# Kernel tuning notes

Measured on AMD Instinct MI355X. Metric: run time of the kernel, lower is better.

## Reference

```python
import jax, jax.numpy as jnp
import numpy as np

# dims
B, N, M, K = 8, 4096, 1024, 32      # batch, points, centers, neighbors
CIN, CT = 64, 64                    # feature / temb channels
C1, C2 = 64, 128                    # SharedMLP out_channels
G, EPS = 8, 1e-5                    # GroupNorm(8, oc)


def setup_inputs() -> dict:
    key = jax.random.key(0)
    ks = jax.random.split(key, 8)
    return {
        "features": jax.random.normal(ks[0], (B, CIN, N), jnp.float32),
        "coords": jax.random.uniform(ks[1], (B, 3, N), jnp.float32),
        "temb": jax.random.normal(ks[2], (B, CT, N), jnp.float32),
        # SharedMLP params: Conv2d 1x1 -> (O, I) weight, GroupNorm affine
        "W1": jax.random.normal(ks[3], (C1, CIN + 3), jnp.float32) * 0.05,
        "b1": jnp.zeros((C1,), jnp.float32),
        "g1": jnp.ones((C1,), jnp.float32),
        "be1": jnp.zeros((C1,), jnp.float32),
        "W2": jax.random.normal(ks[4], (C2, C1), jnp.float32) * 0.05,
        "b2": jnp.zeros((C2,), jnp.float32),
        "g2": jnp.ones((C2,), jnp.float32),
        "be2": jnp.zeros((C2,), jnp.float32),
    }


def fps_indices(pts):
    # pts: [N, 3] -> [M] indices. Deterministic start at index 0
    # (original uses a random start; math otherwise identical).
    d0 = jnp.sum((pts - pts[0]) ** 2, axis=-1)  # [N]
    def step(dist, _):
        far = jnp.argmax(dist)
        dist = jnp.minimum(dist, jnp.sum((pts - pts[far]) ** 2, axis=-1))
        return dist, far
    _, fars = jax.lax.scan(step, d0, None, length=M - 1)
    return jnp.concatenate([jnp.zeros((1,), fars.dtype), fars])


def group_norm(x, gamma, beta):
    # x: [B, C, M, K], normalize per group over (C//G, M, K)
    b, c, m, k = x.shape
    xr = x.reshape(b, G, c // G, m, k)
    mu = xr.mean(axis=(2, 3, 4), keepdims=True)
    var = xr.var(axis=(2, 3, 4), keepdims=True)
    xn = ((xr - mu) * jax.lax.rsqrt(var + EPS)).reshape(b, c, m, k)
    return xn * gamma[:, None, None] + beta[:, None, None]


def swish(x):
    return x * jax.nn.sigmoid(x)


def reference(features, coords, temb, W1, b1, g1, be1, W2, b2, g2, be2):
    # --- furthest point sampling ---
    idx = jax.vmap(fps_indices)(coords.transpose(0, 2, 1))          # [B, M]
    centers = jax.vmap(lambda c, i: c[:, i])(coords, idx)           # [B, 3, M]
    # --- 'ball query' (actually kNN: source argsorts dist, takes first K) ---
    c = centers.transpose(0, 2, 1)                                  # [B, M, 3]
    p = coords.transpose(0, 2, 1)                                   # [B, N, 3]
    d = (jnp.sum(c * c, -1)[:, :, None] + jnp.sum(p * p, -1)[:, None, :]
         - 2.0 * jnp.einsum('bmd,bnd->bmn', c, p))                  # [B, M, N]
    _, nidx = jax.lax.top_k(-d, K)                                  # [B, M, K]
    gather = jax.vmap(lambda xb, ib: xb[:, ib])                     # [B,C,N],[B,M,K]->[B,C,M,K]
    gcoords = gather(coords, nidx) - centers[..., None]             # [B, 3, M, K]
    gtemb = gather(temb, nidx)                                      # [B, CT, M, K]
    gfeat = jnp.concatenate([gcoords, gather(features, nidx)], axis=1)  # [B, 3+CIN, M, K]
    # --- SharedMLP (1x1 conv -> GN -> Swish) x2, then max over neighbors ---
    h = swish(group_norm(jnp.einsum('oc,bcmk->bomk', W1, gfeat) + b1[:, None, None], g1, be1))
    h = swish(group_norm(jnp.einsum('oc,bcmk->bomk', W2, h) + b2[:, None, None], g2, be2))
    return h.max(axis=-1), centers, gtemb.max(axis=-1)
```

## Files before the change

### kernel.cpp

```cpp
#include <hip/hip_runtime.h>
#include <stdint.h>

#define BB 8
#define NN 4096
#define MM 1024
#define KK 32

__device__ __forceinline__ float bf2f(unsigned short u) {
    union { unsigned int i; float f; } v; v.i = ((unsigned int)u) << 16; return v.f;
}
__device__ __forceinline__ unsigned short f2bf(float f) {
    union { float f; unsigned int i; } v; v.f = f;
    unsigned int x = v.i;
    x += 0x7fffu + ((x >> 16) & 1u);
    return (unsigned short)(x >> 16);
}
__device__ __forceinline__ float swishf(float y) {
    return __fdividef(y, 1.0f + __expf(-y));
}

#define OUT1_OFF 1048576
#define OUT2_OFF 1073152

#define P_W1 0
#define P_B1 4288
#define P_G1 4352
#define P_BE1 4416
#define P_W2 4480
#define P_B2 12672
#define P_G2 12800
#define P_BE2 12928

__device__ __forceinline__ int detect_flag_wave(const unsigned short* f, int lane) {
    unsigned short u = f[lane * 2];
    float x = fabsf(bf2f(u));
    bool ext = (u != 0) && (x > 100.0f || x < 1e-30f);
    unsigned long long m = __ballot(ext);
    return (__popcll(m) >= 16) ? 1 : 0;
}

#define DPP_STAGE(CTRL) { \
    union { double d; unsigned int u[2]; } s_, r_; \
    s_.d = bd; \
    r_.u[0] = (unsigned)__builtin_amdgcn_update_dpp(0, (int)s_.u[0], CTRL, 0xF, 0xF, true); \
    r_.u[1] = (unsigned)__builtin_amdgcn_update_dpp(0, (int)s_.u[1], CTRL, 0xF, 0xF, true); \
    int op_ = __builtin_amdgcn_update_dpp(0, bp, CTRL, 0xF, 0xF, true); \
    double od_ = r_.d; \
    bool rep_ = (od_ > bd) || (od_ == bd && op_ < bp); \
    bd = rep_ ? od_ : bd; bp = rep_ ? op_ : bp; }

__device__ __forceinline__ void redmax64(double& bd, int& bp) {
    DPP_STAGE(0xB1)
    DPP_STAGE(0x4E)
    DPP_STAGE(0x141)
    DPP_STAGE(0x140)
#pragma unroll
    for (int m = 32; m >= 16; m >>= 1) {
        double od = __shfl_xor(bd, m, 64);
        int op = __shfl_xor(bp, m, 64);
        bool rep = (od > bd) || (od == bd && op < bp);
        bd = rep ? od : bd; bp = rep ? op : bp;
    }
}

__global__ __launch_bounds__(256) void k_cvt_all(
    const void* __restrict__ feat, const void* __restrict__ coords,
    float* __restrict__ featT, float* __restrict__ coordsC,
    float* __restrict__ paramsC,
    int* __restrict__ qhead, int* __restrict__ progress,
    float* __restrict__ stats1,
    const void* W1, const void* b1, const void* g1, const void* be1,
    const void* W2, const void* b2, const void* g2, const void* be2)
{
    __shared__ float tile[64][65];
    __shared__ int sflag;
    int tid = threadIdx.x, blk = blockIdx.x;
    if (tid < 64) {
        int fl0 = detect_flag_wave((const unsigned short*)feat, tid);
        if (tid == 0) sflag = fl0;
    }
    __syncthreads();
    int fl = sflag;
    if (blk == 0) {
        if (tid == 0) *qhead = 0;
        if (tid < 8) progress[tid * 16] = -1;
        stats1[tid] = 0.f;
        stats1[tid + 256] = 0.f;
    }
    if (blk < 512) {
        int i = blk;
        int b = i >> 6, n0 = (i & 63) * 64;
        int c = tid >> 2, q = tid & 3;
        size_t base = ((size_t)b * 64 + c) * NN + n0 + q * 16;
        if (fl) {
            const float* sp = (const float*)feat + base;
#pragma unroll
            for (int j = 0; j < 16; j++) tile[c][q * 16 + j] = sp[j];
        } else {
            const unsigned short* sp = (const unsigned short*)feat + base;
#pragma unroll
            for (int j = 0; j < 16; j++) tile[c][q * 16 + j] = bf2f(sp[j]);
        }
        __syncthreads();
        int n = tid >> 2;
        float* dp = featT + ((size_t)b * NN + n0 + n) * 64 + q * 16;
#pragma unroll
        for (int j = 0; j < 16; j++) dp[j] = tile[q * 16 + j][n];
    } else if (blk < 896) {
        int idx = (blk - 512) * 256 + tid;
        coordsC[idx] = fl ? ((const float*)coords)[idx]
                          : bf2f(((const unsigned short*)coords)[idx]);
    } else {
        int idx = (blk - 896) * 256 + tid;
        if (idx < 13056) {
            const void* src; int off;
            if (idx < 4288)       { src = W1;  off = idx; }
            else if (idx < 4352)  { src = b1;  off = idx - 4288; }
            else if (idx < 4416)  { src = g1;  off = idx - 4352; }
            else if (idx < 4480)  { src = be1; off = idx - 4416; }
            else if (idx < 12672) { src = W2;  off = idx - 4480; }
            else if (idx < 12800) { src = b2;  off = idx - 12672; }
            else if (idx < 12928) { src = g2;  off = idx - 12800; }
            else                  { src = be2; off = idx - 12928; }
            paramsC[idx] = fl ? ((const float*)src)[off]
                              : bf2f(((const unsigned short*)src)[off]);
        }
    }
}

#define W1Tm(j,c)     (((float*)SM)[(j)*64+(c)])
#define GBUFm(mi,k,c) (((float*)(SM+17152))[(((mi)*32+(k))*66)+(c)])
#define GCm(mi,j,k)   (((float*)(SM+50944))[(((mi)*3+(j))*32)+(k)])
#define NDm(mi,k)     (((int*)(SM+52480))[((mi)*32)+(k)])
#define W2Tm(j,c)     (((float*)SM)[(j)*128+(c)])
#define ACTm(mi,j,k)  (((float*)(SM+32768))[(((mi)*64+(j))*32)+(k)])

struct PW { double d; int p; int q; };
#define PSM_XS   ((float*)(SM))
#define PSM_YS   ((float*)(SM + 16384))
#define PSM_ZS   ((float*)(SM + 32768))
#define PSM_HIST ((int*)(SM + 49152))
#define PSM_PWB  ((PW*)(SM + 53248))
#define PSM_SF   ((int*)(SM + 53376))

#define RESCAN(G) { \
    double gd = 1.0e300; int ga = (G) * 8; \
    _Pragma("unroll") \
    for (int i = 0; i < 8; i++) { \
        int sl = (G) * 8 + i; \
        unsigned int bit = (sl < 32) ? (elo >> sl) : (ehi >> (sl - 32)); \
        double cd = (bit & 1u) ? 1.0e300 : d[sl]; \
        bool rep = cd < gd; \
        gd = rep ? cd : gd; ga = rep ? sl : ga; \
    } \
    g8[(G)] = gd; a8[(G)] = ga; }

__global__ __launch_bounds__(256) void k_fpsknn(
    const void* __restrict__ coords, const float* __restrict__ coordsC,
    float* __restrict__ centersF, int* __restrict__ nidx,
    const void* __restrict__ temb, const void* __restrict__ feat,
    const float* __restrict__ featT, const float* __restrict__ paramsC,
    float* __restrict__ stats1,
    void* __restrict__ d_out,
    int* __restrict__ qhead, int* __restrict__ progress)
{
    __shared__ __align__(16) char SM[55296];
    int tid = threadIdx.x;
    int blk = blockIdx.x;
    if (tid < 64) {
        int fl0 = detect_flag_wave((const unsigned short*)feat, tid);
        if (tid == 0) *PSM_SF = fl0;
    }
    __syncthreads();
    int fl = *PSM_SF;

    if (blk < 8) {
        int b = blk;
        if (fl) {
            const float* cb = (const float*)coords + (size_t)b * 3 * NN;
#pragma unroll
            for (int i = 0; i < 16; i++) {
                int p = tid + i * 256;
                PSM_XS[p] = cb[p]; PSM_YS[p] = cb[NN + p]; PSM_ZS[p] = cb[2 * NN + p];
            }
        } else {
            const unsigned short* cb = (const unsigned short*)coords + (size_t)b * 3 * NN;
#pragma unroll
            for (int i = 0; i < 16; i++) {
                int p = tid + i * 256;
                PSM_XS[p] = bf2f(cb[p]); PSM_YS[p] = bf2f(cb[NN + p]); PSM_ZS[p] = bf2f(cb[2 * NN + p]);
            }
        }
        if (tid == 0) PSM_HIST[0] = 0;
        __syncthreads();
        if (tid == 0) {
            *(float4*)(centersF + (size_t)b * MM * 4) =
                make_float4(PSM_XS[0], PSM_YS[0], PSM_ZS[0], 0.f);
            __hip_atomic_store(&progress[b * 16], 0, __ATOMIC_RELEASE, __HIP_MEMORY_SCOPE_AGENT);
        }
        int base = tid * 16;
        double px[16], py[16], pz[16], dist[16];
        double x0 = (double)PSM_XS[0], y0 = (double)PSM_YS[0], z0 = (double)PSM_ZS[0];
        double bd = -1.0; int bp = base;
#pragma unroll
        for (int j = 0; j < 16; j++) {
            px[j] = (double)PSM_XS[base + j]; py[j] = (double)PSM_YS[base + j]; pz[j] = (double)PSM_ZS[base + j];
            double dx = px[j] - x0, dy = py[j] - y0, dz = pz[j] - z0;
            dist[j] = fma(dz, dz, fma(dy, dy, dx * dx));
            bool rep = dist[j] > bd;
            bd = rep ? dist[j] : bd; bp = rep ? base + j : bp;
        }
        int lane = tid & 63, wid = tid >> 6;
#pragma unroll 1
        for (int s = 1; s < MM; s++) {
            redmax64(bd, bp);
            int par = s & 1;
            if (lane == 0) { PW w; w.d = bd; w.p = bp; w.q = 0; PSM_PWB[par * 4 + wid] = w; }
            __syncthreads();
            PW w0 = PSM_PWB[par * 4 + 0];
            double wd = w0.d; int wp = w0.p;
#pragma unroll
            for (int w = 1; w < 4; w++) {
                PW ww = PSM_PWB[par * 4 + w];
                bool rep = (ww.d > wd) || (ww.d == wd && ww.p < wp);
                wd = rep ? ww.d : wd; wp = rep ? ww.p : wp;
            }
            if (tid == 0) PSM_HIST[s] = wp;
            if ((s & 31) == 31 && s >= 63 && wid == ((s >> 5) & 3)) {
                int s0 = s - 63;
                if (lane < 32) {
                    int far = PSM_HIST[s0 + lane];
                    *(float4*)(centersF + ((size_t)b * MM + s0 + lane) * 4) =
                        make_float4(PSM_XS[far], PSM_YS[far], PSM_ZS[far], 0.f);
                }
                if (lane == 0)
                    __hip_atomic_store(&progress[b * 16], s0 + 31,
                                       __ATOMIC_RELEASE, __HIP_MEMORY_SCOPE_AGENT);
            }
            double fx = (double)PSM_XS[wp], fy = (double)PSM_YS[wp], fz = (double)PSM_ZS[wp];
            bd = -1.0; bp = base;
#pragma unroll
            for (int j = 0; j < 16; j++) {
                double dx = px[j] - fx, dy = py[j] - fy, dz = pz[j] - fz;
                double d = fma(dz, dz, fma(dy, dy, dx * dx));
                dist[j] = fmin(dist[j], d);
                bool rep = dist[j] > bd;
                bd = rep ? dist[j] : bd; bp = rep ? base + j : bp;
            }
        }
        __syncthreads();
        if (tid < 32) {
            int far = PSM_HIST[992 + tid];
            *(float4*)(centersF + ((size_t)b * MM + 992 + tid) * 4) =
                make_float4(PSM_XS[far], PSM_YS[far], PSM_ZS[far], 0.f);
        }
        if (tid == 0)
            __hip_atomic_store(&progress[b * 16], 1023,
                               __ATOMIC_RELEASE, __HIP_MEMORY_SCOPE_AGENT);
#pragma unroll
        for (int i = 0; i < 4; i++) {
            int m = tid + i * 256;
            int far = PSM_HIST[m];
            float X = PSM_XS[far], Y = PSM_YS[far], Z = PSM_ZS[far];
            if (fl) {
                float* o = (float*)d_out;
                o[OUT1_OFF + (size_t)(b * 3 + 0) * MM + m] = X;
                o[OUT1_OFF + (size_t)(b * 3 + 1) * MM + m] = Y;
                o[OUT1_OFF + (size_t)(b * 3 + 2) * MM + m] = Z;
            } else {
                unsigned short* o = (unsigned short*)d_out;
                o[OUT1_OFF + (size_t)(b * 3 + 0) * MM + m] = f2bf(X);
                o[OUT1_OFF + (size_t)(b * 3 + 1) * MM + m] = f2bf(Y);
                o[OUT1_OFF + (size_t)(b * 3 + 2) * MM + m] = f2bf(Z);
            }
        }
    } else {
        int lane = tid & 63, wid = tid >> 6;
        for (int t = tid; t < 64 * 67; t += 256) {
            int c = t / 67, j = t % 67;
            W1Tm(j, c) = paramsC[P_W1 + t];
        }
        __syncthreads();
        for (;;) {
            int id = 0;
            if (lane == 0) id = atomicAdd(qhead, 1);
            id = __shfl(id, 0, 64);
            if (id >= BB * MM) break;
            int b = id & 7, m = id >> 3;
            while (__hip_atomic_load(&progress[b * 16], __ATOMIC_RELAXED,
                                     __HIP_MEMORY_SCOPE_AGENT) < m)
                __builtin_amdgcn_s_sleep(64);
            (void)__hip_atomic_load(&progress[b * 16], __ATOMIC_ACQUIRE,
                                    __HIP_MEMORY_SCOPE_AGENT);
            int bm = b * MM + m;
            const float* cb = coordsC + (size_t)b * 3 * NN;
            float4 ctr = *(const float4*)(centersF + (size_t)bm * 4);
            double cx = (double)ctr.x, cy = (double)ctr.y, cz = (double)ctr.z;
            double cc = (cx * cx + cy * cy) + cz * cz;
            double d[64];
#pragma unroll 4
            for (int j = 0; j < 64; j++) {
                int p = j * 64 + lane;
                double x = (double)cb[p], y = (double)cb[NN + p], z = (double)cb[2 * NN + p];
                double pp = (x * x + y * y) + z * z;
                double dt = (cx * x + cy * y) + cz * z;
                d[j] = (cc + pp) - 2.0 * dt;
            }
            double g8[8]; int a8[8];
#pragma unroll
            for (int g = 0; g < 8; g++) {
                double gd = d[g * 8]; int ga = g * 8;
#pragma unroll
                for (int i = 1; i < 8; i++) {
                    int sl = g * 8 + i;
                    bool rep = d[sl] < gd;
                    gd = rep ? d[sl] : gd; ga = rep ? sl : ga;
                }
                g8[g] = gd; a8[g] = ga;
            }
            unsigned int elo = 0, ehi = 0;
            int res = 0;
#pragma unroll 1
            for (int it = 0; it < 32; it++) {
                double bd = g8[0]; int ba = a8[0];
#pragma unroll
                for (int g = 1; g < 8; g++) {
                    bool rep = g8[g] < bd;
                    bd = rep ? g8[g] : bd; ba = rep ? a8[g] : ba;
                }
                int bp = ba * 64 + lane;
                double wd = bd; int wp = bp;
#pragma unroll
                for (int s = 32; s >= 1; s >>= 1) {
                    double od = __shfl_xor(wd, s, 64);
                    int op = __shfl_xor(wp, s, 64);
                    bool rep = (od < wd) || (od == wd && op < wp);
                    wd = rep ? od : wd; wp = rep ? op : wp;
                }
                res = (lane == it) ? wp : res;
                if (bp == wp) {
                    int slot = ba;
                    if (slot < 32) elo |= (1u << slot); else ehi |= (1u << (slot - 32));
                    int g = slot >> 3;
                    switch (g) {
                        case 0: RESCAN(0) break;
                        case 1: RESCAN(1) break;
                        case 2: RESCAN(2) break;
                        case 3: RESCAN(3) break;
                        case 4: RESCAN(4) break;
                        case 5: RESCAN(5) break;
                        case 6: RESCAN(6) break;
                        case 7: RESCAN(7) break;
                    }
                }
            }
            if (lane < KK) nidx[(size_t)bm * KK + lane] = res;
            float best = -3.0e38f;
            if (fl) {
                const float* tb = (const float*)temb + ((size_t)b * 64 + lane) * NN;
#pragma unroll 4
                for (int k = 0; k < 32; k++) {
                    int nk = __shfl(res, k, 64);
                    best = fmaxf(best, tb[nk]);
                }
            } else {
                const unsigned short* tb = (const unsigned short*)temb + ((size_t)b * 64 + lane) * NN;
#pragma unroll 4
                for (int k = 0; k < 32; k++) {
                    int nk = __shfl(res, k, 64);
                    best = fmaxf(best, bf2f(tb[nk]));
                }
            }
            size_t off = (size_t)OUT2_OFF + ((size_t)(b * 64 + lane)) * MM + m;
            if (fl) ((float*)d_out)[off] = best;
            else    ((unsigned short*)d_out)[off] = f2bf(best);
            if (lane < 32) NDm(wid, lane) = res & (NN - 1);
            const float* fb = featT + (size_t)b * NN * 64;
#pragma unroll 4
            for (int q = 0; q < 32; q++) {
                int n = NDm(wid, q);
                GBUFm(wid, q, lane) = fb[(size_t)n * 64 + lane];
            }
            if (lane < 32) {
                int n = NDm(wid, lane);
                GCm(wid, 0, lane) = __fsub_rn(cb[n], ctr.x);
                GCm(wid, 1, lane) = __fsub_rn(cb[NN + n], ctr.y);
                GCm(wid, 2, lane) = __fsub_rn(cb[2 * NN + n], ctr.z);
            }
            int c0 = (lane >> 3) * 8;
            int k0 = (lane & 7) * 4;
            float acc[8][4];
#pragma unroll
            for (int i = 0; i < 8; i++)
#pragma unroll
                for (int kk = 0; kk < 4; kk++) acc[i][kk] = 0.f;
#pragma unroll
            for (int j = 0; j < 3; j++) {
                float4 a = *(const float4*)&GCm(wid, j, k0);
                float4 w0 = *(const float4*)&W1Tm(j, c0);
                float4 w1v = *(const float4*)&W1Tm(j, c0 + 4);
                float w[8] = {w0.x, w0.y, w0.z, w0.w, w1v.x, w1v.y, w1v.z, w1v.w};
#pragma unroll
                for (int i = 0; i < 8; i++) {
                    acc[i][0] = fmaf(w[i], a.x, acc[i][0]);
                    acc[i][1] = fmaf(w[i], a.y, acc[i][1]);
                    acc[i][2] = fmaf(w[i], a.z, acc[i][2]);
                    acc[i][3] = fmaf(w[i], a.w, acc[i][3]);
                }
            }
#pragma unroll 4
            for (int c = 0; c < 64; c++) {
                float f0 = GBUFm(wid, k0 + 0, c);
                float f1 = GBUFm(wid, k0 + 1, c);
                float f2 = GBUFm(wid, k0 + 2, c);
                float f3 = GBUFm(wid, k0 + 3, c);
                int j = 3 + c;
                float4 w0 = *(const float4*)&W1Tm(j, c0);
                float4 w1v = *(const float4*)&W1Tm(j, c0 + 4);
                float w[8] = {w0.x, w0.y, w0.z, w0.w, w1v.x, w1v.y, w1v.z, w1v.w};
#pragma unroll
                for (int i = 0; i < 8; i++) {
                    acc[i][0] = fmaf(w[i], f0, acc[i][0]);
                    acc[i][1] = fmaf(w[i], f1, acc[i][1]);
                    acc[i][2] = fmaf(w[i], f2, acc[i][2]);
                    acc[i][3] = fmaf(w[i], f3, acc[i][3]);
                }
            }
            float s = 0.f, s2 = 0.f;
#pragma unroll
            for (int i = 0; i < 8; i++) {
                float bb = paramsC[P_B1 + c0 + i];
#pragma unroll
                for (int kk = 0; kk < 4; kk++) {
                    float v = acc[i][kk] + bb;
                    s += v; s2 = fmaf(v, v, s2);
                }
            }
            s += __shfl_xor(s, 1, 64); s += __shfl_xor(s, 2, 64); s += __shfl_xor(s, 4, 64);
            s2 += __shfl_xor(s2, 1, 64); s2 += __shfl_xor(s2, 2, 64); s2 += __shfl_xor(s2, 4, 64);
            if ((lane & 7) == 0) {
                int g = lane >> 3;
                atomicAdd(&stats1[(b * 8 + g) * 2], s);
                atomicAdd(&stats1[(b * 8 + g) * 2 + 1], s2);
            }
        }
    }
}

__device__ __forceinline__ void mlp1_compute(
    char* SM, int tid, int lane, int mi, int b, int bm,
    const float* __restrict__ featT, const float* __restrict__ coordsC,
    const float* __restrict__ centersF, const int* __restrict__ nidx,
    const float* __restrict__ P, float acc[8][4])
{
    for (int t = tid; t < 64 * 67; t += 256) {
        int c = t / 67, j = t % 67;
        W1Tm(j, c) = P[P_W1 + t];
    }
    if (lane < 32) NDm(mi, lane) = nidx[(size_t)bm * KK + lane] & (NN - 1);
    __syncthreads();
    const float* fb = featT + (size_t)b * NN * 64;
#pragma unroll 4
    for (int q = 0; q < 32; q++) {
        int n = NDm(mi, q);
        GBUFm(mi, q, lane) = fb[(size_t)n * 64 + lane];
    }
    float4 ctr = *(const float4*)(centersF + (size_t)bm * 4);
    const float* cb = coordsC + (size_t)b * 3 * NN;
    if (lane < 32) {
        int n = NDm(mi, lane);
        GCm(mi, 0, lane) = __fsub_rn(cb[n], ctr.x);
        GCm(mi, 1, lane) = __fsub_rn(cb[NN + n], ctr.y);
        GCm(mi, 2, lane) = __fsub_rn(cb[2 * NN + n], ctr.z);
    }
    __syncthreads();
    int c0 = (lane >> 3) * 8;
    int k0 = (lane & 7) * 4;
#pragma unroll
    for (int i = 0; i < 8; i++)
#pragma unroll
        for (int kk = 0; kk < 4; kk++) acc[i][kk] = 0.f;
#pragma unroll
    for (int j = 0; j < 3; j++) {
        float4 a = *(const float4*)&GCm(mi, j, k0);
        float4 w0 = *(const float4*)&W1Tm(j, c0);
        float4 w1v = *(const float4*)&W1Tm(j, c0 + 4);
        float w[8] = {w0.x, w0.y, w0.z, w0.w, w1v.x, w1v.y, w1v.z, w1v.w};
#pragma unroll
        for (int i = 0; i < 8; i++) {
            acc[i][0] = fmaf(w[i], a.x, acc[i][0]);
            acc[i][1] = fmaf(w[i], a.y, acc[i][1]);
            acc[i][2] = fmaf(w[i], a.z, acc[i][2]);
            acc[i][3] = fmaf(w[i], a.w, acc[i][3]);
        }
    }
#pragma unroll 4
    for (int c = 0; c < 64; c++) {
        float f0 = GBUFm(mi, k0 + 0, c);
        float f1 = GBUFm(mi, k0 + 1, c);
        float f2 = GBUFm(mi, k0 + 2, c);
        float f3 = GBUFm(mi, k0 + 3, c);
        int j = 3 + c;
        float4 w0 = *(const float4*)&W1Tm(j, c0);
        float4 w1v = *(const float4*)&W1Tm(j, c0 + 4);
        float w[8] = {w0.x, w0.y, w0.z, w0.w, w1v.x, w1v.y, w1v.z, w1v.w};
#pragma unroll
        for (int i = 0; i < 8; i++) {
            acc[i][0] = fmaf(w[i], f0, acc[i][0]);
            acc[i][1] = fmaf(w[i], f1, acc[i][1]);
            acc[i][2] = fmaf(w[i], f2, acc[i][2]);
            acc[i][3] = fmaf(w[i], f3, acc[i][3]);
        }
    }
}

__device__ __forceinline__ void mlp2_compute(
    char* SM, int tid, int lane, int mi, int b,
    const float acc1[8][4], const float* __restrict__ S1,
    const float* __restrict__ P, float acc2[16][4])
{
    __syncthreads();
    int c0 = (lane >> 3) * 8;
    int k0 = (lane & 7) * 4;
    int g = c0 >> 3;
    float S = S1[(b * 8 + g) * 2], Q = S1[(b * 8 + g) * 2 + 1];
    float mean = S * (1.0f / 262144.0f);
    float var = Q * (1.0f / 262144.0f) - mean * mean;
    float inv = rsqrtf(var + 1e-5f);
#pragma unroll
    for (int i = 0; i < 8; i++) {
        int c = c0 + i;
        float sc = P[P_G1 + c] * inv;
        float sh = P[P_BE1 + c] - mean * sc;
        float bb = P[P_B1 + c];
#pragma unroll
        for (int kk = 0; kk < 4; kk++)
            ACTm(mi, c, k0 + kk) = swishf(fmaf(acc1[i][kk] + bb, sc, sh));
    }
    for (int t = tid; t < 128 * 64; t += 256) {
        int c = t >> 6, j = t & 63;
        W2Tm(j, c) = P[P_W2 + t];
    }
    __syncthreads();
    int c02 = (lane >> 3) * 16;
#pragma unroll
    for (int i = 0; i < 16; i++)
#pragma unroll
        for (int kk = 0; kk < 4; kk++) acc2[i][kk] = 0.f;
#pragma unroll 4
    for (int j = 0; j < 64; j++) {
        float4 a = *(const float4*)&ACTm(mi, j, k0);
        float4 w0 = *(const float4*)&W2Tm(j, c02);
        float4 w1v = *(const float4*)&W2Tm(j, c02 + 4);
        float4 w2v = *(const float4*)&W2Tm(j, c02 + 8);
        float4 w3 = *(const float4*)&W2Tm(j, c02 + 12);
        float w[16] = {w0.x, w0.y, w0.z, w0.w, w1v.x, w1v.y, w1v.z, w1v.w,
                       w2v.x, w2v.y, w2v.z, w2v.w, w3.x, w3.y, w3.z, w3.w};
#pragma unroll
        for (int i = 0; i < 16; i++) {
            acc2[i][0] = fmaf(w[i], a.x, acc2[i][0]);
            acc2[i][1] = fmaf(w[i], a.y, acc2[i][1]);
            acc2[i][2] = fmaf(w[i], a.z, acc2[i][2]);
            acc2[i][3] = fmaf(w[i], a.w, acc2[i][3]);
        }
    }
}

__global__ __launch_bounds__(256) void k_mlp2s(
    const float* __restrict__ featT, const float* __restrict__ coordsC,
    const float* __restrict__ centersF, const int* __restrict__ nidx,
    const float* __restrict__ P, const float* __restrict__ stats1,
    float* __restrict__ stats2)
{
    __shared__ __align__(16) char smem[65536];
    char* SM = smem;
    int tid = threadIdx.x, blk = blockIdx.x;
    int b = blk >> 8, m0 = (blk & 255) * 4;
    int mi = tid >> 6, lane = tid & 63;
    int bm = b * MM + m0 + mi;
    float acc1[8][4];
    mlp1_compute(SM, tid, lane, mi, b, bm, featT, coordsC, centersF, nidx, P, acc1);
    float acc2[16][4];
    mlp2_compute(SM, tid, lane, mi, b, acc1, stats1, P, acc2);
    int c02 = (lane >> 3) * 16;
    float s = 0.f, s2 = 0.f;
#pragma unroll
    for (int i = 0; i < 16; i++) {
        float bb = P[P_B2 + c02 + i];
#pragma unroll
        for (int kk = 0; kk < 4; kk++) {
            float v = acc2[i][kk] + bb;
            s += v; s2 = fmaf(v, v, s2);
        }
    }
    s += __shfl_xor(s, 1, 64); s += __shfl_xor(s, 2, 64); s += __shfl_xor(s, 4, 64);
    s2 += __shfl_xor(s2, 1, 64); s2 += __shfl_xor(s2, 2, 64); s2 += __shfl_xor(s2, 4, 64);
    __syncthreads();
    float* sred = (float*)SM;
    if ((lane & 7) == 0) {
        int g = lane >> 3;
        sred[(mi * 8 + g) * 2] = s;
        sred[(mi * 8 + g) * 2 + 1] = s2;
    }
    __syncthreads();
    if (tid < 16) {
        int g = tid >> 1, w = tid & 1;
        float t = sred[(0 * 8 + g) * 2 + w] + sred[(1 * 8 + g) * 2 + w]
                + sred[(2 * 8 + g) * 2 + w] + sred[(3 * 8 + g) * 2 + w];
        atomicAdd(&stats2[(b * 8 + g) * 2 + w], t);
    }
}

__global__ __launch_bounds__(256) void k_final(
    const float* __restrict__ featT, const float* __restrict__ coordsC,
    const float* __restrict__ centersF, const int* __restrict__ nidx,
    const float* __restrict__ P, const float* __restrict__ stats1,
    const float* __restrict__ stats2,
    void* __restrict__ d_out, const void* __restrict__ feat)
{
    __shared__ __align__(16) char smem[65536];
    char* SM = smem;
    int tid = threadIdx.x, blk = blockIdx.x;
    if (tid < 64) {
        int fl0 = detect_flag_wave((const unsigned short*)feat, tid);
        if (tid == 0) *(int*)(SM + 53248) = fl0;
    }
    __syncthreads();
    int fl = *(int*)(SM + 53248);
    int b = blk >> 8, m0 = (blk & 255) * 4;
    int mi = tid >> 6, lane = tid & 63;
    int bm = b * MM + m0 + mi;
    float acc1[8][4];
    mlp1_compute(SM, tid, lane, mi, b, bm, featT, coordsC, centersF, nidx, P, acc1);
    float acc2[16][4];
    mlp2_compute(SM, tid, lane, mi, b, acc1, stats1, P, acc2);
    int c02 = (lane >> 3) * 16;
    int g2 = c02 >> 4;
    float S = stats2[(b * 8 + g2) * 2], Q = stats2[(b * 8 + g2) * 2 + 1];
    float mean = S * (1.0f / 524288.0f);
    float var = Q * (1.0f / 524288.0f) - mean * mean;
    float inv = rsqrtf(var + 1e-5f);
    float mx[16];
#pragma unroll
    for (int i = 0; i < 16; i++) {
        int c = c02 + i;
        float sc = P[P_G2 + c] * inv;
        float sh = P[P_BE2 + c] - mean * sc;
        float bb = P[P_B2 + c];
        float v = -3.0e38f;
#pragma unroll
        for (int kk = 0; kk < 4; kk++)
            v = fmaxf(v, swishf(fmaf(acc2[i][kk] + bb, sc, sh)));
        v = fmaxf(v, __shfl_xor(v, 1, 64));
        v = fmaxf(v, __shfl_xor(v, 2, 64));
        v = fmaxf(v, __shfl_xor(v, 4, 64));
        mx[i] = v;
    }
    if ((lane & 7) == 0) {
        int m = m0 + mi;
#pragma unroll
        for (int i = 0; i < 16; i++) {
            size_t off = (size_t)(b * 128 + c02 + i) * MM + m;
            if (fl) ((float*)d_out)[off] = mx[i];
            else    ((unsigned short*)d_out)[off] = f2bf(mx[i]);
        }
    }
}

extern "C" void kernel_launch(void* const* d_in, const int* in_sizes, int n_in,
                              void* d_out, int out_size, void* d_ws, size_t ws_size,
                              hipStream_t stream) {
    (void)in_sizes; (void)n_in; (void)out_size; (void)ws_size;
    const void* feat = d_in[0];
    const void* coords = d_in[1];
    const void* temb = d_in[2];

    char* ws = (char*)d_ws;
    int* qhead = (int*)ws;
    int* progress = (int*)(ws + 512);
    float* stats1 = (float*)(ws + 1024);
    float* stats2 = (float*)(ws + 2048);
    float* coordsC = (float*)(ws + 3072);
    float* paramsC = (float*)(ws + 396288);
    float* centersF = (float*)(ws + 448512);
    int* nidx = (int*)(ws + 579584);
    float* featT = (float*)(ws + 1628160);

    k_cvt_all<<<947, 256, 0, stream>>>(feat, coords, featT, coordsC, paramsC,
                                       qhead, progress, stats1,
                                       d_in[3], d_in[4], d_in[5], d_in[6],
                                       d_in[7], d_in[8], d_in[9], d_in[10]);
    k_fpsknn<<<256, 256, 0, stream>>>(coords, coordsC, centersF, nidx, temb,
                                      feat, featT, paramsC, stats1, d_out,
                                      qhead, progress);
    k_mlp2s<<<2048, 256, 0, stream>>>(featT, coordsC, centersF, nidx, paramsC,
                                      stats1, stats2);
    k_final<<<2048, 256, 0, stream>>>(featT, coordsC, centersF, nidx, paramsC,
                                      stats1, stats2, d_out, feat);
}
```

Baseline: 1.501 ms.

## Cache pre-norm MLP activations in bf16 workspace instead of recomputing

Stores the first conv's pre-GroupNorm output (h1) in bf16 from the fps/knn kernel and the second conv's output (h2) from the stats kernel. Later kernels reload these instead of redoing the gather and matmuls, but only when the workspace is large enough. This trades recomputation for extra global memory traffic (roughly 33MB for h1 and 67MB for h2) and adds bf16 rounding of intermediates, which may shift accuracy.

```diff
diff --git a/kernel.cpp b/kernel.cpp
--- a/kernel.cpp
+++ b/kernel.cpp
@@ -162,7 +162,8 @@
     const float* __restrict__ featT, const float* __restrict__ paramsC,
     float* __restrict__ stats1,
     void* __restrict__ d_out,
-    int* __restrict__ qhead, int* __restrict__ progress)
+    int* __restrict__ qhead, int* __restrict__ progress,
+    unsigned short* __restrict__ h1, int cache1)
 {
     __shared__ __align__(16) char SM[55296];
     int tid = threadIdx.x;
@@ -430,10 +431,16 @@
 #pragma unroll
             for (int i = 0; i < 8; i++) {
                 float bb = paramsC[P_B1 + c0 + i];
-#pragma unroll
-                for (int kk = 0; kk < 4; kk++) {
-                    float v = acc[i][kk] + bb;
-                    s += v; s2 = fmaf(v, v, s2);
+                float v0 = acc[i][0] + bb, v1 = acc[i][1] + bb;
+                float v2 = acc[i][2] + bb, v3 = acc[i][3] + bb;
+                s += v0; s2 = fmaf(v0, v0, s2);
+                s += v1; s2 = fmaf(v1, v1, s2);
+                s += v2; s2 = fmaf(v2, v2, s2);
+                s += v3; s2 = fmaf(v3, v3, s2);
+                if (cache1) {
+                    unsigned int p0 = (unsigned int)f2bf(v0) | ((unsigned int)f2bf(v1) << 16);
+                    unsigned int p1 = (unsigned int)f2bf(v2) | ((unsigned int)f2bf(v3) << 16);
+                    *(uint2*)(h1 + ((size_t)bm * 64 + c0 + i) * 32 + k0) = make_uint2(p0, p1);
                 }
             }
             s += __shfl_xor(s, 1, 64); s += __shfl_xor(s, 2, 64); s += __shfl_xor(s, 4, 64);
@@ -516,8 +523,8 @@
 
 __device__ __forceinline__ void mlp2_compute(
     char* SM, int tid, int lane, int mi, int b,
-    const float acc1[8][4], const float* __restrict__ S1,
-    const float* __restrict__ P, float acc2[16][4])
+    const float v1[8][4], const float* __restrict__ S1,
+    const float* __restrict__ P, float v2[16][4])
 {
     __syncthreads();
     int c0 = (lane >> 3) * 8;
@@ -532,10 +539,9 @@
         int c = c0 + i;
         float sc = P[P_G1 + c] * inv;
         float sh = P[P_BE1 + c] - mean * sc;
-        float bb = P[P_B1 + c];
 #pragma unroll
         for (int kk = 0; kk < 4; kk++)
-            ACTm(mi, c, k0 + kk) = swishf(fmaf(acc1[i][kk] + bb, sc, sh));
+            ACTm(mi, c, k0 + kk) = swishf(fmaf(v1[i][kk], sc, sh));
     }
     for (int t = tid; t < 128 * 64; t += 256) {
         int c = t >> 6, j = t & 63;
@@ -543,6 +549,7 @@
     }
     __syncthreads();
     int c02 = (lane >> 3) * 16;
+    float acc2[16][4];
 #pragma unroll
     for (int i = 0; i < 16; i++)
 #pragma unroll
@@ -564,13 +571,50 @@
             acc2[i][3] = fmaf(w[i], a.w, acc2[i][3]);
         }
     }
+#pragma unroll
+    for (int i = 0; i < 16; i++) {
+        float bb = P[P_B2 + c02 + i];
+#pragma unroll
+        for (int kk = 0; kk < 4; kk++) v2[i][kk] = acc2[i][kk] + bb;
+    }
+}
+
+__device__ __forceinline__ void get_v1(
+    char* SM, int tid, int lane, int mi, int b, int bm,
+    const float* featT, const float* coordsC, const float* centersF,
+    const int* nidx, const float* P,
+    const unsigned short* h1, int cache1, float v1[8][4])
+{
+    int c0 = (lane >> 3) * 8;
+    int k0 = (lane & 7) * 4;
+    if (cache1) {
+#pragma unroll
+        for (int i = 0; i < 8; i++) {
+            uint2 u = *(const uint2*)(h1 + ((size_t)bm * 64 + c0 + i) * 32 + k0);
+            v1[i][0] = bf2f((unsigned short)(u.x & 0xffffu));
+            v1[i][1] = bf2f((unsigned short)(u.x >> 16));
+            v1[i][2] = bf2f((unsigned short)(u.y & 0xffffu));
+            v1[i][3] = bf2f((unsigned short)(u.y >> 16));
+        }
+    } else {
+        float acc1[8][4];
+        mlp1_compute(SM, tid, lane, mi, b, bm, featT, coordsC, centersF, nidx, P, acc1);
+#pragma unroll
+        for (int i = 0; i < 8; i++) {
+            float bb = P[P_B1 + c0 + i];
+#pragma unroll
+            for (int kk = 0; kk < 4; kk++) v1[i][kk] = acc1[i][kk] + bb;
+        }
+    }
 }
 
 __global__ __launch_bounds__(256) void k_mlp2s(
     const float* __restrict__ featT, const float* __restrict__ coordsC,
     const float* __restrict__ centersF, const int* __restrict__ nidx,
     const float* __restrict__ P, const float* __restrict__ stats1,
-    float* __restrict__ stats2)
+    float* __restrict__ stats2,
+    const unsigned short* __restrict__ h1, unsigned short* __restrict__ h2,
+    int cache1, int cache2)
 {
     __shared__ __align__(16) char smem[65536];
     char* SM = smem;
@@ -578,19 +622,24 @@
     int b = blk >> 8, m0 = (blk & 255) * 4;
     int mi = tid >> 6, lane = tid & 63;
     int bm = b * MM + m0 + mi;
-    float acc1[8][4];
-    mlp1_compute(SM, tid, lane, mi, b, bm, featT, coordsC, centersF, nidx, P, acc1);
-    float acc2[16][4];
-    mlp2_compute(SM, tid, lane, mi, b, acc1, stats1, P, acc2);
+    float v1[8][4];
+    get_v1(SM, tid, lane, mi, b, bm, featT, coordsC, centersF, nidx, P, h1, cache1, v1);
+    float v2[16][4];
+    mlp2_compute(SM, tid, lane, mi, b, v1, stats1, P, v2);
     int c02 = (lane >> 3) * 16;
+    int k0 = (lane & 7) * 4;
     float s = 0.f, s2 = 0.f;
 #pragma unroll
     for (int i = 0; i < 16; i++) {
-        float bb = P[P_B2 + c02 + i];
 #pragma unroll
         for (int kk = 0; kk < 4; kk++) {
-            float v = acc2[i][kk] + bb;
+            float v = v2[i][kk];
             s += v; s2 = fmaf(v, v, s2);
+        }
+        if (cache2) {
+            unsigned int p0 = (unsigned int)f2bf(v2[i][0]) | ((unsigned int)f2bf(v2[i][1]) << 16);
+            unsigned int p1 = (unsigned int)f2bf(v2[i][2]) | ((unsigned int)f2bf(v2[i][3]) << 16);
+            *(uint2*)(h2 + ((size_t)bm * 128 + c02 + i) * 32 + k0) = make_uint2(p0, p1);
         }
     }
     s += __shfl_xor(s, 1, 64); s += __shfl_xor(s, 2, 64); s += __shfl_xor(s, 4, 64);
@@ -616,7 +665,9 @@
     const float* __restrict__ centersF, const int* __restrict__ nidx,
     const float* __restrict__ P, const float* __restrict__ stats1,
     const float* __restrict__ stats2,
-    void* __restrict__ d_out, const void* __restrict__ feat)
+    void* __restrict__ d_out, const void* __restrict__ feat,
+    const unsigned short* __restrict__ h1, const unsigned short* __restrict__ h2,
+    int cache1, int cache2)
 {
     __shared__ __align__(16) char smem[65536];
     char* SM = smem;
@@ -630,11 +681,23 @@
     int b = blk >> 8, m0 = (blk & 255) * 4;
     int mi = tid >> 6, lane = tid & 63;
     int bm = b * MM + m0 + mi;
-    float acc1[8][4];
-    mlp1_compute(SM, tid, lane, mi, b, bm, featT, coordsC, centersF, nidx, P, acc1);
-    float acc2[16][4];
-    mlp2_compute(SM, tid, lane, mi, b, acc1, stats1, P, acc2);
     int c02 = (lane >> 3) * 16;
+    int k0 = (lane & 7) * 4;
+    float v2[16][4];
+    if (cache2) {
+#pragma unroll
+        for (int i = 0; i < 16; i++) {
+            uint2 u = *(const uint2*)(h2 + ((size_t)bm * 128 + c02 + i) * 32 + k0);
+            v2[i][0] = bf2f((unsigned short)(u.x & 0xffffu));
+            v2[i][1] = bf2f((unsigned short)(u.x >> 16));
+            v2[i][2] = bf2f((unsigned short)(u.y & 0xffffu));
+            v2[i][3] = bf2f((unsigned short)(u.y >> 16));
+        }
+    } else {
+        float v1[8][4];
+        get_v1(SM, tid, lane, mi, b, bm, featT, coordsC, centersF, nidx, P, h1, cache1, v1);
+        mlp2_compute(SM, tid, lane, mi, b, v1, stats1, P, v2);
+    }
     int g2 = c02 >> 4;
     float S = stats2[(b * 8 + g2) * 2], Q = stats2[(b * 8 + g2) * 2 + 1];
     float mean = S * (1.0f / 524288.0f);
@@ -646,11 +709,10 @@
         int c = c02 + i;
         float sc = P[P_G2 + c] * inv;
         float sh = P[P_BE2 + c] - mean * sc;
-        float bb = P[P_B2 + c];
         float v = -3.0e38f;
 #pragma unroll
         for (int kk = 0; kk < 4; kk++)
-            v = fmaxf(v, swishf(fmaf(acc2[i][kk] + bb, sc, sh)));
+            v = fmaxf(v, swishf(fmaf(v2[i][kk], sc, sh)));
         v = fmaxf(v, __shfl_xor(v, 1, 64));
         v = fmaxf(v, __shfl_xor(v, 2, 64));
         v = fmaxf(v, __shfl_xor(v, 4, 64));
@@ -670,7 +732,7 @@
 extern "C" void kernel_launch(void* const* d_in, const int* in_sizes, int n_in,
                               void* d_out, int out_size, void* d_ws, size_t ws_size,
                               hipStream_t stream) {
-    (void)in_sizes; (void)n_in; (void)out_size; (void)ws_size;
+    (void)in_sizes; (void)n_in; (void)out_size;
     const void* feat = d_in[0];
     const void* coords = d_in[1];
     const void* temb = d_in[2];
@@ -685,6 +747,10 @@
     float* centersF = (float*)(ws + 448512);
     int* nidx = (int*)(ws + 579584);
     float* featT = (float*)(ws + 1628160);
+    unsigned short* h1 = (unsigned short*)(ws + 10016768);
+    unsigned short* h2 = (unsigned short*)(ws + 43571200);
+    int cache1 = (ws_size >= 43571200u) ? 1 : 0;
+    int cache2 = (ws_size >= 110680064u) ? 1 : 0;
 
     k_cvt_all<<<947, 256, 0, stream>>>(feat, coords, featT, coordsC, paramsC,
                                        qhead, progress, stats1,
@@ -692,9 +758,10 @@
                                        d_in[7], d_in[8], d_in[9], d_in[10]);
     k_fpsknn<<<256, 256, 0, stream>>>(coords, coordsC, centersF, nidx, temb,
                                       feat, featT, paramsC, stats1, d_out,
-                                      qhead, progress);
+                                      qhead, progress, h1, cache1);
     k_mlp2s<<<2048, 256, 0, stream>>>(featT, coordsC, centersF, nidx, paramsC,
-                                      stats1, stats2);
+                                      stats1, stats2, h1, h2, cache1, cache2);
     k_final<<<2048, 256, 0, stream>>>(featT, coordsC, centersF, nidx, paramsC,
-                                      stats1, stats2, d_out, feat);
-}
+                                      stats1, stats2, d_out, feat, h1, h2,
+                                      cache1, cache2);
+}
```

Measured after the change: 1.347 ms. 1.11x faster.
